# Optimization experiments

Hardware: AMD Instinct MI355X
Metric: run time of the kernel (lower is better)

## Reference

```python
import jax, jax.numpy as jnp
import numpy as np

T_SIM = 32  # simulation_length


def _uniform_spikes(rates, cycle, T):
    """Port of to_uniform_spikes: place round(rate*T) evenly spaced spikes over T cycles."""
    Ns = jnp.round(rates * T).astype(jnp.int32)
    mask = (Ns != 0) & (Ns != T) & (cycle < T)
    N_safe = jnp.maximum(Ns, 1)
    spacing = T / N_safe.astype(rates.dtype)
    cyc = jnp.asarray(cycle, rates.dtype)
    res = mask & (jnp.floor(cyc / spacing) < N_safe.astype(rates.dtype)) & (jnp.floor(jnp.mod(cyc, spacing)) == 0)
    res = res.astype(rates.dtype)
    return jnp.where(Ns == T, jnp.asarray(1.0, rates.dtype), res)


def setup_inputs() -> dict:
    key = jax.random.key(0)
    k1, k2 = jax.random.split(key)
    B, N, C = 256, 2048, 8
    x = jax.random.uniform(k1, (B, N), dtype=jnp.float32)          # preprocessed rates in [0,1]
    W = jax.random.normal(k2, (C, N, N), dtype=jnp.float32) * 0.02  # core_matrix per core, (n_in, n_out)
    thresholds = jnp.ones((C,), dtype=jnp.float32)
    return {"x": x, "W": W, "thresholds": thresholds}


def reference(x, W, thresholds):
    """Spiking simulation of a chain of C cores over T cycles.

    Core c has latency c; core 0 reads input spikes, core c reads core c-1's
    previous-cycle buffer; output counts accumulate the last core's buffer.
    """
    T = T_SIM
    dtype = x.dtype
    B, N = x.shape
    C = W.shape[0]
    lat = jnp.arange(C)  # per-core pipeline latency (chain topology)

    # input spike train (T, B, N), padded with (C-1) zero cycles (post-T input is zeros)
    train = jax.vmap(lambda c: _uniform_spikes(x, c, T))(jnp.arange(T))
    train = jnp.concatenate([train, jnp.zeros((C - 1, B, N), dtype)], axis=0)

    thr = thresholds[:, None, None]  # (C,1,1)

    def step(carry, input_spikes):
        memb, buf, counts, cycle = carry
        # gather phase: all cores read prior-cycle buffers / current input spikes
        signals = jnp.concatenate([input_spikes[None], buf[:-1]], axis=0)  # (C,B,N)
        active = (cycle >= lat) & (cycle < T + lat)  # (C,)
        am = active[:, None, None]
        # integrate: memb += signals @ core_matrix (only for active cores)
        delta = jnp.einsum('cbi,cio->cbo', signals, W)
        memb2 = memb + jnp.where(am, delta, jnp.asarray(0.0, dtype))
        # fire: thresholding_mode '<'  ->  fired = (threshold < memb)
        fired = thr < memb2
        buf2 = jnp.where(am, fired.astype(dtype), buf)
        # firing_mode 'Default': subtract threshold from fired membranes
        memb3 = jnp.where(am & fired, memb2 - thr, memb2)
        counts2 = counts + buf2[-1]  # output spans = last core's full buffer
        return (memb3, buf2, counts2, cycle + 1), None

    init = (jnp.zeros((C, B, N), dtype),
            jnp.zeros((C, B, N), dtype),
            jnp.zeros((B, N), dtype),
            jnp.int32(0))
    (_, _, counts, _), _ = jax.lax.scan(step, init, train)
    # spike counts -> rates
    return counts / T
```

## Files before the change

### kernel.cpp

```cpp
#include <hip/hip_runtime.h>
#include <stdint.h>

#define NN 2048
#define NCORE 8
#define TSIM 32
#define PLANE (256*2048)

typedef int i4v __attribute__((ext_vector_type(4)));

__device__ __forceinline__ void load_lds16(const void* g, void* l) {
  __builtin_amdgcn_global_load_lds((const __attribute__((address_space(1))) void*)g,
                                   (__attribute__((address_space(3))) void*)l, 16, 0, 0);
}

__global__ void zero_f32_kernel(float* __restrict__ p, int n4) {
  int i = blockIdx.x * 256 + threadIdx.x;
  if (i < n4) ((float4*)p)[i] = make_float4(0.f, 0.f, 0.f, 0.f);
}

__global__ void spikes_kernel(const float* __restrict__ x, uint8_t* __restrict__ strain) {
  int gid = blockIdx.x * 256 + threadIdx.x;
  int b = gid >> 7, kg = gid & 127;
  const float* xp = x + (size_t)b * NN + kg * 16;
  float nsf[16], sp[16]; int ns[16];
#pragma unroll
  for (int e = 0; e < 16; ++e) {
    float nv = rintf(xp[e] * 32.0f);
    nsf[e] = nv; ns[e] = (int)nv; sp[e] = 32.0f / fmaxf(nv, 1.0f);
  }
  uint32_t dst = (uint32_t)b * 2048 + ((uint32_t)(kg >> 2) << 6)
               + ((uint32_t)((kg & 3) ^ ((b >> 1) & 3)) << 4);
  int cyc0 = blockIdx.y * 4;
#pragma unroll
  for (int i = 0; i < 4; ++i) {
    int cyc = cyc0 + i;
    float ct = (float)cyc;
    uint32_t w[4] = {0u, 0u, 0u, 0u};
#pragma unroll
    for (int e = 0; e < 16; ++e) {
      bool res;
      if (ns[e] == TSIM)      res = true;
      else if (ns[e] == 0)    res = false;
      else {
        float q = floorf(ct / sp[e]);
        float m = fmodf(ct, sp[e]);
        res = (q < nsf[e]) && (floorf(m) == 0.0f);
      }
      if (res) w[e >> 2] |= 1u << ((e & 3) * 8);
    }
    uint4 pk; pk.x = w[0]; pk.y = w[1]; pk.z = w[2]; pk.w = w[3];
    *(uint4*)(strain + (size_t)cyc * PLANE + dst) = pk;
  }
}

__global__ __launch_bounds__(256) void wsplit_kernel(const float* __restrict__ W,
                                                     uint8_t* __restrict__ Whm) {
  __shared__ uint32_t lds[3 * 2048];
  int kk = blockIdx.x, nt = blockIdx.y, c = blockIdx.z;
  int tid = threadIdx.x, lane = tid & 63, wid = tid >> 6;
  const float* src = W + ((size_t)c * NN + (size_t)kk * 128) * NN + nt * 64 + lane;
#pragma unroll
  for (int kp = 0; kp < 8; ++kp) {
    uint32_t pk0 = 0, pk1 = 0, pk2 = 0;
#pragma unroll
    for (int q = 0; q < 4; ++q) {
      int kl = kp * 16 + wid * 4 + q;
      float w = src[(size_t)kl * NN];
      int wi = (int)rintf(w * 0x1p25f);
      int l8 = (int)(int8_t)(uint8_t)(wi & 0xFF);
      int r1 = (wi - l8) >> 8;
      int m8 = (int)(int8_t)(uint8_t)(r1 & 0xFF);
      int h8 = (r1 - m8) >> 8;
      pk0 |= ((uint32_t)(uint8_t)h8) << (q * 8);
      pk1 |= ((uint32_t)(uint8_t)m8) << (q * 8);
      pk2 |= ((uint32_t)(uint8_t)l8) << (q * 8);
    }
    int kq = kp * 4 + wid;
    lds[0 * 2048 + kq * 64 + lane] = pk0;
    lds[1 * 2048 + kq * 64 + lane] = pk1;
    lds[2 * 2048 + kq * 64 + lane] = pk2;
  }
  __syncthreads();
  size_t chunkbase = (((size_t)c * 32 + nt) * 16 + kk) * 24576;
#pragma unroll
  for (int g = 0; g < 6; ++g) {
    int idx = g * 256 + tid;
    int ks2 = (idx >= 768) ? 1 : 0;
    int rem = idx - ks2 * 768;
    int p = rem >> 8;
    int n = (rem >> 2) & 63;
    int s = rem & 3;
    int k16 = s ^ ((n >> 1) & 3);
    int kqb = ks2 * 16 + k16 * 4;
    uint4 v;
    v.x = lds[p * 2048 + (kqb + 0) * 64 + n];
    v.y = lds[p * 2048 + (kqb + 1) * 64 + n];
    v.z = lds[p * 2048 + (kqb + 2) * 64 + n];
    v.w = lds[p * 2048 + (kqb + 3) * 64 + n];
    *(uint4*)(Whm + chunkbase + (size_t)idx * 16) = v;
  }
}

__global__ __launch_bounds__(512, 4) void step4_kernel(
    const uint8_t* __restrict__ Whm, const float* __restrict__ thresholds,
    const uint8_t* __restrict__ strain, uint8_t* bufs,
    float* __restrict__ memb, float* __restrict__ out, int j, int c_lo) {
  __shared__ uint8_t smem[57344];

  const int tid = threadIdx.x;
  const int c = c_lo + blockIdx.x;
  const int yy = blockIdx.y;
  const int nt = yy & 31, rq = yy >> 5;
  const int sl = 4 * (j - c);
  const int l = tid & 63, wid = tid >> 6;
  const int wm = wid >> 2, wn = wid & 3;
  const int lr = l & 15, lh = l >> 4;

  const uint8_t* pls[4];
#pragma unroll
  for (int st = 0; st < 4; ++st)
    pls[st] = (c == 0) ? strain + (size_t)(sl + st) * PLANE
                       : bufs + ((size_t)(c - 1) * 8 + ((sl + st) & 7)) * PLANE;

  const uint8_t* ab[2];
  uint32_t adst[2];
#pragma unroll
  for (int j_ = 0; j_ < 2; ++j_) {
    int gi = j_ * 512 + tid;
    int si = gi >> 8, idx = gi & 255;
    int row = idx >> 2, kq = idx & 3;
    ab[j_] = pls[si] + (size_t)(rq * 64 + row) * 2048 + kq * 16;
    adst[j_] = si * 8192 + idx * 16;
  }
  const uint8_t* wbase = Whm + (((size_t)c * 32 + nt) * 16) * 24576;
  uint8_t* Bs = smem + 32768;

  const uint32_t swz = (uint32_t)(lh ^ ((lr >> 1) & 3)) << 4;
  const uint32_t aoff = (uint32_t)(wm * 32 + lr) * 64 + swz;
  const uint32_t boff = (uint32_t)(wn * 16 + lr) * 64 + swz;

  i4v acc[4][3][2];
  const i4v izero = {0, 0, 0, 0};
#pragma unroll
  for (int st = 0; st < 4; ++st)
#pragma unroll
    for (int p = 0; p < 3; ++p) { acc[st][p][0] = izero; acc[st][p][1] = izero; }

  auto issue = [&](int k, int slot) {
#pragma unroll
    for (int j_ = 0; j_ < 2; ++j_)
      load_lds16(ab[j_] + k * 64, smem + adst[j_] + slot * 4096);
    const uint8_t* bs = wbase + (size_t)(k >> 1) * 24576 + (size_t)(k & 1) * 12288;
    uint8_t* Bd = Bs + slot * 12288;
    load_lds16(bs + tid * 16, Bd + tid * 16);
    if (tid < 256) load_lds16(bs + 8192 + tid * 16, Bd + 8192 + tid * 16);
  };

  auto comp = [&](int slot) {
    const uint8_t* Bb = Bs + slot * 12288;
    i4v bf0 = *(const i4v*)(Bb + 0 * 4096 + boff);
    i4v bf1 = *(const i4v*)(Bb + 1 * 4096 + boff);
    i4v bf2 = *(const i4v*)(Bb + 2 * 4096 + boff);
    __builtin_amdgcn_s_setprio(1);
#pragma unroll
    for (int st = 0; st < 4; ++st) {
      const uint8_t* Ab = smem + st * 8192 + slot * 4096;
#pragma unroll
      for (int mi = 0; mi < 2; ++mi) {
        i4v a_ = *(const i4v*)(Ab + aoff + mi * 1024);
        acc[st][0][mi] = __builtin_amdgcn_mfma_i32_16x16x64_i8(a_, bf0, acc[st][0][mi], 0, 0, 0);
        acc[st][1][mi] = __builtin_amdgcn_mfma_i32_16x16x64_i8(a_, bf1, acc[st][1][mi], 0, 0, 0);
        acc[st][2][mi] = __builtin_amdgcn_mfma_i32_16x16x64_i8(a_, bf2, acc[st][2][mi], 0, 0, 0);
      }
    }
    __builtin_amdgcn_s_setprio(0);
  };

#define WAITV(n) asm volatile("s_waitcnt vmcnt(" #n ")" ::: "memory")
#define WAITL() asm volatile("s_waitcnt lgkmcnt(0)" ::: "memory")
#define BAR() do { __builtin_amdgcn_s_barrier(); __builtin_amdgcn_sched_barrier(0); } while (0)

  issue(0, 0);
  for (int k = 0; k < 32; ++k) {
    if (k < 31) {
      issue(k + 1, (k + 1) & 1);
      if (tid < 256) { WAITV(4); } else { WAITV(3); }
    } else {
      WAITV(0);
    }
    BAR();
    comp(k & 1);
    WAITL();
    BAR();
  }
#undef WAITV
#undef WAITL
#undef BAR

  const float thr = thresholds[c];
  float* Cl = (float*)smem;
  float4 d[4][2];
#pragma unroll
  for (int st = 0; st < 4; ++st) {
    __syncthreads();
#pragma unroll
    for (int mi = 0; mi < 2; ++mi)
#pragma unroll
      for (int rg = 0; rg < 4; ++rg) {
        int row = wm * 32 + mi * 16 + lh * 4 + rg;
        int col = wn * 16 + lr;
        int di = (acc[st][0][mi][rg] << 16) + (acc[st][1][mi][rg] << 8) + acc[st][2][mi][rg];
        Cl[row * 68 + col] = (float)di * 0x1p-25f;
      }
    __syncthreads();
#pragma unroll
    for (int p = 0; p < 2; ++p) {
      int rr = p * 32 + (tid >> 4);
      int c4 = (tid & 15) * 4;
      d[st][p] = *(const float4*)&Cl[rr * 68 + c4];
    }
  }

  float* membp = memb + (size_t)c * PLANE;
  uint8_t* bps[4];
#pragma unroll
  for (int st = 0; st < 4; ++st)
    bps[st] = bufs + ((size_t)c * 8 + ((sl + st) & 7)) * PLANE;
  const bool last = (j == 14);
#pragma unroll
  for (int p = 0; p < 2; ++p) {
    int rr = p * 32 + (tid >> 4);
    int c4 = (tid & 15) * 4;
    int b = rq * 64 + rr;
    int o = nt * 64 + c4;
    size_t idx = (size_t)b * NN + o;
    float4 mv = *(float4*)(membp + idx);
    float4 cv;
    if (c == 7) cv = *(float4*)(out + idx);
    uint32_t ba = (uint32_t)b * 2048 + ((uint32_t)(o >> 6) << 6)
                + ((uint32_t)(((o >> 4) & 3) ^ ((b >> 1) & 3)) << 4) + (o & 15);
#pragma unroll
    for (int st = 0; st < 4; ++st) {
      mv.x += d[st][p].x; mv.y += d[st][p].y; mv.z += d[st][p].z; mv.w += d[st][p].w;
      bool fx = thr < mv.x, fy = thr < mv.y, fz = thr < mv.z, fw = thr < mv.w;
      if (fx) mv.x -= thr;  if (fy) mv.y -= thr;
      if (fz) mv.z -= thr;  if (fw) mv.w -= thr;
      if (c < 7) {
        uchar4 pk;
        pk.x = fx ? 1 : 0; pk.y = fy ? 1 : 0; pk.z = fz ? 1 : 0; pk.w = fw ? 1 : 0;
        *(uchar4*)(bps[st] + ba) = pk;
      } else {
        cv.x += fx ? 1.f : 0.f; cv.y += fy ? 1.f : 0.f;
        cv.z += fz ? 1.f : 0.f; cv.w += fw ? 1.f : 0.f;
      }
    }
    *(float4*)(membp + idx) = mv;
    if (c == 7) {
      if (last) { cv.x *= 0x1p-5f; cv.y *= 0x1p-5f; cv.z *= 0x1p-5f; cv.w *= 0x1p-5f; }
      *(float4*)(out + idx) = cv;
    }
  }
}

extern "C" void kernel_launch(void* const* d_in, const int* in_sizes, int n_in,
                              void* d_out, int out_size, void* d_ws, size_t ws_size,
                              hipStream_t stream) {
  const float* x   = (const float*)d_in[0];
  const float* W   = (const float*)d_in[1];
  const float* thr = (const float*)d_in[2];
  float* out = (float*)d_out;
  uint8_t* ws = (uint8_t*)d_ws;

  float*   memb   = (float*)ws;
  uint8_t* strain = ws + 16777216;
  uint8_t* bufs   = ws + 33554432;
  uint8_t* Whm    = ws + 62914560;

  zero_f32_kernel<<<dim3(4096), 256, 0, stream>>>(memb, 1048576);
  zero_f32_kernel<<<dim3(512),  256, 0, stream>>>(out, 131072);
  spikes_kernel<<<dim3(128, 8), 256, 0, stream>>>(x, strain);
  wsplit_kernel<<<dim3(16, 32, 8), 256, 0, stream>>>(W, Whm);

  for (int j = 0; j < 15; ++j) {
    int c_lo = (j > 7) ? (j - 7) : 0;
    int c_hi = (j < 7) ? j : 7;
    step4_kernel<<<dim3(c_hi - c_lo + 1, 128), 512, 0, stream>>>(
        Whm, thr, strain, bufs, memb, out, j, c_lo);
  }
}
```

Before: 811.5 us.

## Process eight time steps per launch and drop zero-fill kernels

Each step kernel now advances eight cycles per core instead of four, so the wavefront schedule needs 11 launches instead of 15. The spike buffer ring is widened to 16 planes. The tile is reshaped to 64 rows by 32 output columns per block, doubling the grid, and each weight tile fetched is reused across eight time steps. The separate zero-fill kernels for membrane and output are removed; initial state is instead synthesised in the first step of each core. In exchange, LDS use per block grows and accumulator register pressure rises, which may limit occupancy.

```diff
diff --git a/kernel.cpp b/kernel.cpp
--- a/kernel.cpp
+++ b/kernel.cpp
@@ -11,11 +11,6 @@
 __device__ __forceinline__ void load_lds16(const void* g, void* l) {
   __builtin_amdgcn_global_load_lds((const __attribute__((address_space(1))) void*)g,
                                    (__attribute__((address_space(3))) void*)l, 16, 0, 0);
-}
-
-__global__ void zero_f32_kernel(float* __restrict__ p, int n4) {
-  int i = blockIdx.x * 256 + threadIdx.x;
-  if (i < n4) ((float4*)p)[i] = make_float4(0.f, 0.f, 0.f, 0.f);
 }
 
 __global__ void spikes_kernel(const float* __restrict__ x, uint8_t* __restrict__ strain) {
@@ -101,77 +96,69 @@
   }
 }
 
-__global__ __launch_bounds__(512, 4) void step4_kernel(
+__global__ __launch_bounds__(512, 4) void step8_kernel(
     const uint8_t* __restrict__ Whm, const float* __restrict__ thresholds,
     const uint8_t* __restrict__ strain, uint8_t* bufs,
     float* __restrict__ memb, float* __restrict__ out, int j, int c_lo) {
-  __shared__ uint8_t smem[57344];
+  __shared__ uint8_t smem[77824];
 
   const int tid = threadIdx.x;
   const int c = c_lo + blockIdx.x;
   const int yy = blockIdx.y;
-  const int nt = yy & 31, rq = yy >> 5;
-  const int sl = 4 * (j - c);
+  const int nt64 = yy >> 3, nh = (yy >> 2) & 1, rq = yy & 3;
+  const int sl = 8 * (j - c);
   const int l = tid & 63, wid = tid >> 6;
-  const int wm = wid >> 2, wn = wid & 3;
+  const int wm = wid >> 1, wn = wid & 1;
   const int lr = l & 15, lh = l >> 4;
-
-  const uint8_t* pls[4];
-#pragma unroll
-  for (int st = 0; st < 4; ++st)
-    pls[st] = (c == 0) ? strain + (size_t)(sl + st) * PLANE
-                       : bufs + ((size_t)(c - 1) * 8 + ((sl + st) & 7)) * PLANE;
-
-  const uint8_t* ab[2];
-  uint32_t adst[2];
-#pragma unroll
-  for (int j_ = 0; j_ < 2; ++j_) {
+  uint8_t* Bs = smem + 65536;
+
+  const uint8_t* srcb = (c == 0) ? strain : bufs + (size_t)(c - 1) * 16 * PLANE;
+  const uint8_t* ab[4];
+  uint32_t adst[4];
+#pragma unroll
+  for (int j_ = 0; j_ < 4; ++j_) {
     int gi = j_ * 512 + tid;
     int si = gi >> 8, idx = gi & 255;
     int row = idx >> 2, kq = idx & 3;
-    ab[j_] = pls[si] + (size_t)(rq * 64 + row) * 2048 + kq * 16;
+    int pid = (c == 0) ? (sl + si) : ((sl + si) & 15);
+    ab[j_] = srcb + (size_t)pid * PLANE + (size_t)(rq * 64 + row) * 2048 + kq * 16;
     adst[j_] = si * 8192 + idx * 16;
   }
-  const uint8_t* wbase = Whm + (((size_t)c * 32 + nt) * 16) * 24576;
-  uint8_t* Bs = smem + 32768;
+  const uint8_t* bb = Whm + (((size_t)c * 32 + nt64) * 16) * 24576
+                    + ((size_t)(tid >> 7) * 256 + (size_t)nh * 128 + (tid & 127)) * 16;
 
   const uint32_t swz = (uint32_t)(lh ^ ((lr >> 1) & 3)) << 4;
-  const uint32_t aoff = (uint32_t)(wm * 32 + lr) * 64 + swz;
+  const uint32_t aoff = (uint32_t)(wm * 16 + lr) * 64 + swz;
   const uint32_t boff = (uint32_t)(wn * 16 + lr) * 64 + swz;
 
-  i4v acc[4][3][2];
+  i4v acc[8][3];
   const i4v izero = {0, 0, 0, 0};
 #pragma unroll
-  for (int st = 0; st < 4; ++st)
-#pragma unroll
-    for (int p = 0; p < 3; ++p) { acc[st][p][0] = izero; acc[st][p][1] = izero; }
+  for (int st = 0; st < 8; ++st)
+#pragma unroll
+    for (int p = 0; p < 3; ++p) acc[st][p] = izero;
 
   auto issue = [&](int k, int slot) {
 #pragma unroll
-    for (int j_ = 0; j_ < 2; ++j_)
+    for (int j_ = 0; j_ < 4; ++j_)
       load_lds16(ab[j_] + k * 64, smem + adst[j_] + slot * 4096);
-    const uint8_t* bs = wbase + (size_t)(k >> 1) * 24576 + (size_t)(k & 1) * 12288;
-    uint8_t* Bd = Bs + slot * 12288;
-    load_lds16(bs + tid * 16, Bd + tid * 16);
-    if (tid < 256) load_lds16(bs + 8192 + tid * 16, Bd + 8192 + tid * 16);
+    if (tid < 384)
+      load_lds16(bb + (size_t)(k >> 1) * 24576 + (size_t)(k & 1) * 12288,
+                 Bs + slot * 6144 + tid * 16);
   };
 
   auto comp = [&](int slot) {
-    const uint8_t* Bb = Bs + slot * 12288;
-    i4v bf0 = *(const i4v*)(Bb + 0 * 4096 + boff);
-    i4v bf1 = *(const i4v*)(Bb + 1 * 4096 + boff);
-    i4v bf2 = *(const i4v*)(Bb + 2 * 4096 + boff);
+    const uint8_t* Bb = Bs + slot * 6144;
+    i4v bf0 = *(const i4v*)(Bb + 0 * 2048 + boff);
+    i4v bf1 = *(const i4v*)(Bb + 1 * 2048 + boff);
+    i4v bf2 = *(const i4v*)(Bb + 2 * 2048 + boff);
     __builtin_amdgcn_s_setprio(1);
 #pragma unroll
-    for (int st = 0; st < 4; ++st) {
-      const uint8_t* Ab = smem + st * 8192 + slot * 4096;
-#pragma unroll
-      for (int mi = 0; mi < 2; ++mi) {
-        i4v a_ = *(const i4v*)(Ab + aoff + mi * 1024);
-        acc[st][0][mi] = __builtin_amdgcn_mfma_i32_16x16x64_i8(a_, bf0, acc[st][0][mi], 0, 0, 0);
-        acc[st][1][mi] = __builtin_amdgcn_mfma_i32_16x16x64_i8(a_, bf1, acc[st][1][mi], 0, 0, 0);
-        acc[st][2][mi] = __builtin_amdgcn_mfma_i32_16x16x64_i8(a_, bf2, acc[st][2][mi], 0, 0, 0);
-      }
+    for (int st = 0; st < 8; ++st) {
+      i4v a_ = *(const i4v*)(smem + st * 8192 + slot * 4096 + aoff);
+      acc[st][0] = __builtin_amdgcn_mfma_i32_16x16x64_i8(a_, bf0, acc[st][0], 0, 0, 0);
+      acc[st][1] = __builtin_amdgcn_mfma_i32_16x16x64_i8(a_, bf1, acc[st][1], 0, 0, 0);
+      acc[st][2] = __builtin_amdgcn_mfma_i32_16x16x64_i8(a_, bf2, acc[st][2], 0, 0, 0);
     }
     __builtin_amdgcn_s_setprio(0);
   };
@@ -184,7 +171,7 @@
   for (int k = 0; k < 32; ++k) {
     if (k < 31) {
       issue(k + 1, (k + 1) & 1);
-      if (tid < 256) { WAITV(4); } else { WAITV(3); }
+      if (wid < 6) { WAITV(5); } else { WAITV(4); }
     } else {
       WAITV(0);
     }
@@ -199,66 +186,57 @@
 
   const float thr = thresholds[c];
   float* Cl = (float*)smem;
-  float4 d[4][2];
-#pragma unroll
-  for (int st = 0; st < 4; ++st) {
+  const int err = tid >> 3;
+  const int ec4 = (tid & 7) * 4;
+  float4 d[8];
+#pragma unroll
+  for (int st = 0; st < 8; ++st) {
     __syncthreads();
 #pragma unroll
-    for (int mi = 0; mi < 2; ++mi)
-#pragma unroll
-      for (int rg = 0; rg < 4; ++rg) {
-        int row = wm * 32 + mi * 16 + lh * 4 + rg;
-        int col = wn * 16 + lr;
-        int di = (acc[st][0][mi][rg] << 16) + (acc[st][1][mi][rg] << 8) + acc[st][2][mi][rg];
-        Cl[row * 68 + col] = (float)di * 0x1p-25f;
-      }
+    for (int rg = 0; rg < 4; ++rg) {
+      int row = wm * 16 + lh * 4 + rg;
+      int col = wn * 16 + lr;
+      int di = (acc[st][0][rg] << 16) + (acc[st][1][rg] << 8) + acc[st][2][rg];
+      Cl[row * 36 + col] = (float)di * 0x1p-25f;
+    }
     __syncthreads();
-#pragma unroll
-    for (int p = 0; p < 2; ++p) {
-      int rr = p * 32 + (tid >> 4);
-      int c4 = (tid & 15) * 4;
-      d[st][p] = *(const float4*)&Cl[rr * 68 + c4];
-    }
-  }
-
+    d[st] = *(const float4*)&Cl[err * 36 + ec4];
+  }
+
+  const int b = rq * 64 + err;
+  const int o = nt64 * 64 + nh * 32 + ec4;
+  const size_t idx = (size_t)b * NN + o;
   float* membp = memb + (size_t)c * PLANE;
-  uint8_t* bps[4];
-#pragma unroll
-  for (int st = 0; st < 4; ++st)
-    bps[st] = bufs + ((size_t)c * 8 + ((sl + st) & 7)) * PLANE;
-  const bool last = (j == 14);
-#pragma unroll
-  for (int p = 0; p < 2; ++p) {
-    int rr = p * 32 + (tid >> 4);
-    int c4 = (tid & 15) * 4;
-    int b = rq * 64 + rr;
-    int o = nt * 64 + c4;
-    size_t idx = (size_t)b * NN + o;
-    float4 mv = *(float4*)(membp + idx);
-    float4 cv;
-    if (c == 7) cv = *(float4*)(out + idx);
-    uint32_t ba = (uint32_t)b * 2048 + ((uint32_t)(o >> 6) << 6)
-                + ((uint32_t)(((o >> 4) & 3) ^ ((b >> 1) & 3)) << 4) + (o & 15);
-#pragma unroll
-    for (int st = 0; st < 4; ++st) {
-      mv.x += d[st][p].x; mv.y += d[st][p].y; mv.z += d[st][p].z; mv.w += d[st][p].w;
-      bool fx = thr < mv.x, fy = thr < mv.y, fz = thr < mv.z, fw = thr < mv.w;
-      if (fx) mv.x -= thr;  if (fy) mv.y -= thr;
-      if (fz) mv.z -= thr;  if (fw) mv.w -= thr;
-      if (c < 7) {
-        uchar4 pk;
-        pk.x = fx ? 1 : 0; pk.y = fy ? 1 : 0; pk.z = fz ? 1 : 0; pk.w = fw ? 1 : 0;
-        *(uchar4*)(bps[st] + ba) = pk;
-      } else {
-        cv.x += fx ? 1.f : 0.f; cv.y += fy ? 1.f : 0.f;
-        cv.z += fz ? 1.f : 0.f; cv.w += fw ? 1.f : 0.f;
-      }
-    }
-    *(float4*)(membp + idx) = mv;
-    if (c == 7) {
-      if (last) { cv.x *= 0x1p-5f; cv.y *= 0x1p-5f; cv.z *= 0x1p-5f; cv.w *= 0x1p-5f; }
-      *(float4*)(out + idx) = cv;
-    }
+  float4 mv;
+  if (j == c) mv = make_float4(0.f, 0.f, 0.f, 0.f);
+  else        mv = *(float4*)(membp + idx);
+  float4 cv;
+  if (c == 7) {
+    if (j == 7) cv = make_float4(0.f, 0.f, 0.f, 0.f);
+    else        cv = *(float4*)(out + idx);
+  }
+  const uint32_t ba = (uint32_t)b * 2048 + ((uint32_t)(o >> 6) << 6)
+                    + ((uint32_t)(((o >> 4) & 3) ^ ((b >> 1) & 3)) << 4) + (o & 15);
+#pragma unroll
+  for (int st = 0; st < 8; ++st) {
+    mv.x += d[st].x; mv.y += d[st].y; mv.z += d[st].z; mv.w += d[st].w;
+    bool fx = thr < mv.x, fy = thr < mv.y, fz = thr < mv.z, fw = thr < mv.w;
+    if (fx) mv.x -= thr;  if (fy) mv.y -= thr;
+    if (fz) mv.z -= thr;  if (fw) mv.w -= thr;
+    if (c < 7) {
+      uint8_t* bpl = bufs + ((size_t)c * 16 + ((sl + st) & 15)) * PLANE;
+      uchar4 pk;
+      pk.x = fx ? 1 : 0; pk.y = fy ? 1 : 0; pk.z = fz ? 1 : 0; pk.w = fw ? 1 : 0;
+      *(uchar4*)(bpl + ba) = pk;
+    } else {
+      cv.x += fx ? 1.f : 0.f; cv.y += fy ? 1.f : 0.f;
+      cv.z += fz ? 1.f : 0.f; cv.w += fw ? 1.f : 0.f;
+    }
+  }
+  *(float4*)(membp + idx) = mv;
+  if (c == 7) {
+    if (j == 10) { cv.x *= 0x1p-5f; cv.y *= 0x1p-5f; cv.z *= 0x1p-5f; cv.w *= 0x1p-5f; }
+    *(float4*)(out + idx) = cv;
   }
 }
 
@@ -274,17 +252,15 @@
   float*   memb   = (float*)ws;
   uint8_t* strain = ws + 16777216;
   uint8_t* bufs   = ws + 33554432;
-  uint8_t* Whm    = ws + 62914560;
-
-  zero_f32_kernel<<<dim3(4096), 256, 0, stream>>>(memb, 1048576);
-  zero_f32_kernel<<<dim3(512),  256, 0, stream>>>(out, 131072);
+  uint8_t* Whm    = ws + 92274688;
+
   spikes_kernel<<<dim3(128, 8), 256, 0, stream>>>(x, strain);
   wsplit_kernel<<<dim3(16, 32, 8), 256, 0, stream>>>(W, Whm);
 
-  for (int j = 0; j < 15; ++j) {
-    int c_lo = (j > 7) ? (j - 7) : 0;
+  for (int j = 0; j < 11; ++j) {
+    int c_lo = (j > 3) ? (j - 3) : 0;
     int c_hi = (j < 7) ? j : 7;
-    step4_kernel<<<dim3(c_hi - c_lo + 1, 128), 512, 0, stream>>>(
+    step8_kernel<<<dim3(c_hi - c_lo + 1, 256), 512, 0, stream>>>(
         Whm, thr, strain, bufs, memb, out, j, c_lo);
   }
 }
```

New measurement: 966.6 us. +19.1%, slower.
